# Kernel tuning notes

Measured on AMD Instinct MI355X. Metric: run time of the kernel, lower is better.

## Reference

```python
import jax, jax.numpy as jnp
import numpy as np

# SOLO decoupled-head postprocessing config (TrainConfig)
GRIDS = (40, 36, 24, 16, 12)
STRIDES = (4.0, 8.0, 16.0, 32.0, 64.0)
NMS_PRE = 500
SCORE_THR = 0.1
MASK_THR = 0.005
UPDATE_THR = 0.001
SIGMA = 2.0
MAX_PER_IMG = 100
NUM_CLASSES = 80


def _cell_meta():
    """Per-flattened-cell metadata across the 5 FPN levels (static)."""
    trans_diff, seg_diff, num_grids, strides = [], [], [], []
    t, s = 0, 0
    for g, st in zip(GRIDS, STRIDES):
        n = g * g
        trans_diff.append(np.full(n, t, np.int32))
        seg_diff.append(np.full(n, s, np.int32))
        num_grids.append(np.full(n, g, np.int32))
        strides.append(np.full(n, st, np.float32))
        t += n
        s += g
    return (jnp.asarray(np.concatenate(trans_diff)),
            jnp.asarray(np.concatenate(seg_diff)),
            jnp.asarray(np.concatenate(num_grids)),
            jnp.asarray(np.concatenate(strides)))


def setup_inputs() -> dict:
    key = jax.random.key(0)
    k1, k2, k3 = jax.random.split(key, 3)
    n_cells = sum(g * g for g in GRIDS)   # 3872
    n_rows = sum(GRIDS)                   # 128
    H, W = 200, 304                        # stride-4 map of an 800x1216 image
    return {
        "cate_preds": jax.random.uniform(k1, (n_cells, NUM_CLASSES), jnp.float32),
        "seg_preds_x": jax.random.uniform(k2, (n_rows, H, W), jnp.float32),
        "seg_preds_y": jax.random.uniform(k3, (n_rows, H, W), jnp.float32),
        "ori_h": 427,
        "ori_w": 640,
    }


def _matrix_nms(hardf, labels, scores, sum_masks):
    """Matrix NMS with gaussian decay. hardf: [n, h, w] float, descending scores."""
    n = hardf.shape[0]
    flat = hardf.reshape(n, -1)                      # [n, h*w]
    inter = flat @ flat.T                            # [n, n] pairwise intersection
    union = sum_masks[None, :] + sum_masks[:, None] - inter
    iou = jnp.where(union > 0, inter / jnp.maximum(union, 1e-12), 0.0)
    tri = jnp.triu(jnp.ones((n, n), jnp.float32), 1)  # cols > rows (strict upper)
    same = (labels[None, :] == labels[:, None]) & (labels[:, None] >= 0)
    decay_iou = iou * tri * same.astype(jnp.float32)  # [n, n]
    comp = decay_iou.max(axis=0)                      # max IoU with higher-scored same-class
    decay_m = jnp.exp(-SIGMA * decay_iou ** 2)
    comp_m = jnp.exp(-SIGMA * comp[:, None] ** 2)     # compensate[i, j] = f(comp[i])
    coeff = (decay_m / comp_m).min(axis=0)            # [n]
    return scores * coeff


def reference(cate_preds, seg_preds_x, seg_preds_y, ori_h, ori_w):
    trans_diff, seg_diff, num_grids, strides = _cell_meta()
    C = cate_preds.shape[1]
    flat = cate_preds.reshape(-1)
    flat = jnp.where(flat > SCORE_THR, flat, -1.0)
    scores, idx = jax.lax.top_k(flat, NMS_PRE)        # fixed-size candidate set
    loc = idx // C
    labels = (idx % C).astype(jnp.int32)
    valid = scores > SCORE_THR

    td, sd = trans_diff[loc], seg_diff[loc]
    ng, st = num_grids[loc], strides[loc]
    y_inds = (loc - td) // ng + sd
    x_inds = (loc - td) % ng + sd

    soft = seg_preds_x[x_inds] * seg_preds_y[y_inds]  # [N, H, W]
    hard = soft > MASK_THR
    sum_masks = hard.sum(axis=(1, 2)).astype(jnp.float32)
    keep = valid & (sum_masks > st)
    seg_score = (soft * hard).sum(axis=(1, 2)) / jnp.maximum(sum_masks, 1e-6)
    scores = jnp.where(keep, scores * seg_score, 0.0)
    keepf = keep.astype(jnp.float32)
    hardf = hard.astype(jnp.float32) * keepf[:, None, None]
    sum_masks = sum_masks * keepf
    labels = jnp.where(keep, labels, -1)

    # descending sort (matrix NMS assumes descending scores)
    order = jnp.argsort(-scores)
    scores, labels = scores[order], labels[order]
    soft, hardf, sum_masks = soft[order], hardf[order], sum_masks[order]

    scores = _matrix_nms(hardf, labels, scores, sum_masks)
    scores = jnp.where(scores > UPDATE_THR, scores, 0.0)

    top_scores, top_idx = jax.lax.top_k(scores, MAX_PER_IMG)
    top_soft = soft[top_idx]                          # [100, H, W]
    top_labels = labels[top_idx]

    H, W = top_soft.shape[1], top_soft.shape[2]
    up = jax.image.resize(top_soft, (MAX_PER_IMG, H * 4, W * 4), method="bilinear")
    up = jax.image.resize(up, (MAX_PER_IMG, ori_h, ori_w), method="bilinear")
    seg_masks = (up > MASK_THR).astype(jnp.float32)
    return seg_masks, top_labels, top_scores
```

## Files before the change

### kernel.cpp

```cpp
#include <hip/hip_runtime.h>
#include <stdint.h>

typedef unsigned int u32;
typedef unsigned long long u64;

#define NCELLS  3872
#define NCLS    80
#define NFLAT   309760
#define NPRE    500
#define NPAD    512
#define HH      200
#define WW      304
#define NPIX    60800
#define NWORDS  950
#define MSTRIDE 960
#define MAXOUT  100
#define OH      427
#define OW      640
#define MH      800
#define MW      1216
#define MAXG    4096
#define MAXPAIRS 16384
#define OUT_LBL 27328000
#define OUT_SCR 27328100
#define ROWS_PER_BLK 2
#define NRBLK 214

#define S_THR 0.1f
#define M_THR 0.005f
#define U_THR 0.001f

#define OFF_HIST1   0u
#define OFF_META    263168u
#define ZERO_BYTES  263232u
#define OFF_CAND    263424u
#define OFF_RAW     296192u
#define OFF_LOC     298240u
#define OFF_LABEL   300288u
#define OFF_XIND    302336u
#define OFF_YIND    304384u
#define OFF_STRIDE  306432u
#define OFF_SMF     308480u
#define OFF_SCORE   310528u
#define OFF_LABELK  312576u
#define OFF_ORDER   314624u
#define OFF_SSCORE  316672u
#define OFF_TOPC    318720u
#define OFF_PAIRI   319232u
#define OFF_PAIRIOU 384768u
#define OFF_W1YT0   450304u
#define OFF_W1YA    453504u
#define OFF_W1YB    456704u
#define OFF_W1XT0   459904u
#define OFF_W1XA    464768u
#define OFF_W1XB    469632u
#define OFF_W2YS    474496u
#define OFF_W2YW    476224u
#define OFF_W2XS    483072u
#define OFF_W2XW    485632u
#define OFF_MASKS   495872u
#define OFF_MASKT   4335872u
#define OFF_PARTD   8227072u
#define WS_NEED     12118272u

#define P_U32(off) ((u32*)(ws + (off)))
#define P_I32(off) ((int*)(ws + (off)))
#define P_F32(off) ((float*)(ws + (off)))
#define P_U64(off) ((u64*)(ws + (off)))

__device__ __forceinline__ void levelMeta(int loc, int& td, int& sd, int& ng, float& st) {
  if (loc < 1600)      { td = 0;    sd = 0;   ng = 40; st = 4.f;  }
  else if (loc < 2896) { td = 1600; sd = 40;  ng = 36; st = 8.f;  }
  else if (loc < 3472) { td = 2896; sd = 76;  ng = 24; st = 16.f; }
  else if (loc < 3728) { td = 3472; sd = 100; ng = 16; st = 32.f; }
  else                 { td = 3728; sd = 116; ng = 12; st = 64.f; }
}

__device__ __forceinline__ u32 vbin(float v) {
  int b = (int)(v * 65536.0f);
  if (b > 65535) b = 65535;
  if (b < 0) b = 0;
  return (u32)b;
}

__device__ __forceinline__ u64 shflx64(u64 v, int m) {
  u32 lo = (u32)v, hi = (u32)(v >> 32);
  lo = (u32)__shfl_xor((int)lo, m);
  hi = (u32)__shfl_xor((int)hi, m);
  return (((u64)hi) << 32) | lo;
}

__global__ void kh1(const float* __restrict__ cate, char* __restrict__ ws) {
  int i = blockIdx.x * 256 + threadIdx.x;
  if (i >= NFLAT / 4) return;
  float4 v = ((const float4*)cate)[i];
  u32* h = P_U32(OFF_HIST1);
  if (v.x > S_THR) atomicAdd(&h[vbin(v.x)], 1u);
  if (v.y > S_THR) atomicAdd(&h[vbin(v.y)], 1u);
  if (v.z > S_THR) atomicAdd(&h[vbin(v.z)], 1u);
  if (v.w > S_THR) atomicAdd(&h[vbin(v.w)], 1u);
}

__global__ __launch_bounds__(1024) void kc1(char* __restrict__ ws) {
  __shared__ u32 cs[1024];
  __shared__ u32 sfx[1024];
  __shared__ int cbS;
  __shared__ u32 aboveS;
  int t = threadIdx.x;
  const u32* h = P_U32(OFF_HIST1);
  u32 s = 0;
  for (int b = 0; b < 64; b++) s += h[t * 64 + b];
  cs[t] = s; sfx[t] = s;
  if (t == 0) cbS = -1;
  __syncthreads();
  for (int off = 1; off < 1024; off <<= 1) {
    u32 v = (t + off < 1024) ? sfx[t + off] : 0u;
    __syncthreads();
    sfx[t] += v;
    __syncthreads();
  }
  u32 nxt = (t < 1023) ? sfx[t + 1] : 0u;
  if (sfx[t] >= NPRE && nxt < NPRE) { cbS = t; aboveS = nxt; }
  __syncthreads();
  u32* meta = P_U32(OFF_META);
  if (cbS < 0) {
    if (t == 0) { meta[0] = 0u; meta[1] = sfx[0]; meta[2] = 0u; }
    return;
  }
  int cb = cbS;
  if (t < 64) cs[t] = h[cb * 64 + t];
  __syncthreads();
  if (t == 0) {
    u32 cum = aboveS;
    u32 bin = (u32)(cb * 64);
    for (int b = 63; b >= 0; b--) {
      u32 hb = cs[b];
      if (cum + hb >= NPRE) { bin = (u32)(cb * 64 + b); break; }
      cum += hb;
    }
    meta[0] = bin; meta[1] = cum; meta[2] = bin;
  }
}

__global__ void kg(const float* __restrict__ cate, char* __restrict__ ws) {
  u32 key = P_U32(OFF_META)[2];
  int i = blockIdx.x * 256 + threadIdx.x;
  if (i >= NFLAT / 4) return;
  float4 v = ((const float4*)cate)[i];
  u64* cand = P_U64(OFF_CAND);
  u32* cntp = &P_U32(OFF_META)[3];
  #pragma unroll
  for (int q = 0; q < 4; q++) {
    float f = (q == 0) ? v.x : (q == 1) ? v.y : (q == 2) ? v.z : v.w;
    if (f > S_THR && vbin(f) >= key) {
      u32 pos = atomicAdd(cntp, 1u);
      if (pos < MAXG) cand[pos] = (((u64)__float_as_uint(f)) << 32) | (u32)(~(u32)(i * 4 + q));
    }
  }
}

__global__ __launch_bounds__(1024) void kselw(char* __restrict__ ws) {
  __shared__ u64 sk[MAXG];
  int tid = threadIdx.x;
  int G = (int)P_U32(OFF_META)[3]; if (G > MAXG) G = MAXG;
  int n = NPAD;
  while (n < G) n <<= 1;
  const u64* cand = P_U64(OFF_CAND);
  if (n == NPAD) {
    u64 key = (tid < NPAD) ? ((tid < G) ? cand[tid] : 0ull) : 0ull;
    for (int k = 2; k <= NPAD; k <<= 1) {
      for (int j = k >> 1; j > 0; j >>= 1) {
        bool up = ((tid & k) == 0);
        u64 other;
        if (j < 64) {
          other = shflx64(key, j);
        } else {
          if (tid < NPAD) sk[tid] = key;
          __syncthreads();
          other = sk[(tid ^ j) & (NPAD - 1)];
          __syncthreads();
        }
        bool takeMax = (((tid & j) == 0) == up);
        u64 nk = takeMax ? (key > other ? key : other) : (key < other ? key : other);
        if (tid < NPAD) key = nk;
      }
    }
    if (tid < NPAD) sk[tid] = key;
    __syncthreads();
  } else {
    for (int i = tid; i < n; i += 1024) sk[i] = (i < G) ? cand[i] : 0ull;
    __syncthreads();
    for (int k = 2; k <= n; k <<= 1) {
      for (int j = k >> 1; j > 0; j >>= 1) {
        for (int i = tid; i < n; i += 1024) {
          int l = i ^ j;
          if (l > i) {
            u64 a = sk[i], b = sk[l];
            bool sw = ((i & k) == 0) ? (a < b) : (a > b);
            if (sw) { sk[i] = b; sk[l] = a; }
          }
        }
        __syncthreads();
      }
    }
  }
  if (tid < NPAD) {
    float rawv = -1.f; int loc = 0, lab = -1, xi = 0, yi = 0; float st = 3.0e38f;
    if (tid < NPRE && tid < G) {
      u64 key = sk[tid];
      u32 b = (u32)(key >> 32);
      u32 idx = ~((u32)(key & 0xffffffffu));
      rawv = __uint_as_float(b);
      loc = (int)(idx / (u32)NCLS);
      lab = (int)(idx - (u32)loc * NCLS);
      int td, sd, ng; levelMeta(loc, td, sd, ng, st);
      int rel = loc - td;
      int row = rel / ng;
      yi = row + sd;
      xi = (rel - row * ng) + sd;
    }
    P_F32(OFF_RAW)[tid] = rawv;
    P_I32(OFF_LABEL)[tid] = lab;
    P_I32(OFF_XIND)[tid] = xi;
    P_I32(OFF_YIND)[tid] = yi;
    P_F32(OFF_STRIDE)[tid] = st;
    P_F32(OFF_SCORE)[tid] = 0.f;
    P_I32(OFF_LABELK)[tid] = -1;
    P_F32(OFF_SMF)[tid] = 0.f;
  }
  int t = tid;
  for (int r = t; r < MH; r += 1024) {
    float s1 = ((float)r + 0.5f) * 0.25f - 0.5f;
    int t0 = (int)floorf(s1);
    float f = s1 - (float)t0;
    float wa = 1.f - f, wb = f;
    bool ia = (t0 >= 0) && (t0 < HH);
    bool ib = ((t0 + 1) >= 0) && ((t0 + 1) < HH);
    float tw = (ia ? wa : 0.f) + (ib ? wb : 0.f);
    float na = ia ? (wa / tw) : 0.f;
    float nb = ib ? (wb / tw) : 0.f;
    int base; float A, B;
    if (t0 < 0) { base = 0; A = nb; B = 0.f; }
    else if (t0 >= HH - 1) { base = HH - 2; A = 0.f; B = na; }
    else { base = t0; A = na; B = nb; }
    P_I32(OFF_W1YT0)[r] = base;
    P_F32(OFF_W1YA)[r] = A;
    P_F32(OFF_W1YB)[r] = B;
  }
  for (int c = t; c < MW; c += 1024) {
    float s1 = ((float)c + 0.5f) * 0.25f - 0.5f;
    int t0 = (int)floorf(s1);
    float f = s1 - (float)t0;
    float wa = 1.f - f, wb = f;
    bool ia = (t0 >= 0) && (t0 < WW);
    bool ib = ((t0 + 1) >= 0) && ((t0 + 1) < WW);
    float tw = (ia ? wa : 0.f) + (ib ? wb : 0.f);
    float na = ia ? (wa / tw) : 0.f;
    float nb = ib ? (wb / tw) : 0.f;
    int base; float A, B;
    if (t0 < 0) { base = 0; A = nb; B = 0.f; }
    else if (t0 >= WW - 1) { base = WW - 2; A = 0.f; B = na; }
    else { base = t0; A = na; B = nb; }
    P_I32(OFF_W1XT0)[c] = base;
    P_F32(OFF_W1XA)[c] = A;
    P_F32(OFF_W1XB)[c] = B;
  }
  for (int o = t; o < OH; o += 1024) {
    const float inv = (float)(800.0 / 427.0);
    float s2 = ((float)o + 0.5f) * inv - 0.5f;
    int rA = (int)ceilf(s2 - inv);
    int rB = (int)floorf(s2 + inv);
    if (rA < 0) rA = 0;
    if (rB > MH - 1) rB = MH - 1;
    float tot = 0.f;
    for (int r = rA; r <= rB; r++) {
      float x = fabsf(s2 - (float)r) / inv;
      float w = 1.f - x; if (w < 0.f) w = 0.f;
      tot += w;
    }
    int base = rA; if (base > MH - 4) base = MH - 4;
    float o4[4] = {0.f, 0.f, 0.f, 0.f};
    for (int r = rA; r <= rB; r++) {
      float x = fabsf(s2 - (float)r) / inv;
      float w = 1.f - x; if (w < 0.f) w = 0.f;
      o4[r - base] += w / tot;
    }
    P_I32(OFF_W2YS)[o] = base;
    float* wp = P_F32(OFF_W2YW) + o * 4;
    wp[0] = o4[0]; wp[1] = o4[1]; wp[2] = o4[2]; wp[3] = o4[3];
  }
  for (int o = t; o < OW; o += 1024) {
    const float inv = (float)(1216.0 / 640.0);
    float s2 = ((float)o + 0.5f) * inv - 0.5f;
    int rA = (int)ceilf(s2 - inv);
    int rB = (int)floorf(s2 + inv);
    if (rA < 0) rA = 0;
    if (rB > MW - 1) rB = MW - 1;
    float tot = 0.f;
    for (int r = rA; r <= rB; r++) {
      float x = fabsf(s2 - (float)r) / inv;
      float w = 1.f - x; if (w < 0.f) w = 0.f;
      tot += w;
    }
    int base = rA; if (base > MW - 4) base = MW - 4;
    float o4[4] = {0.f, 0.f, 0.f, 0.f};
    for (int r = rA; r <= rB; r++) {
      float x = fabsf(s2 - (float)r) / inv;
      float w = 1.f - x; if (w < 0.f) w = 0.f;
      o4[r - base] += w / tot;
    }
    P_I32(OFF_W2XS)[o] = base;
    float* wp = P_F32(OFF_W2XW) + o * 4;
    wp[0] = o4[0]; wp[1] = o4[1]; wp[2] = o4[2]; wp[3] = o4[3];
  }
}

__global__ __launch_bounds__(256) void kmaskA(const float* __restrict__ segx, const float* __restrict__ segy,
                                              char* __restrict__ ws) {
  __shared__ float lx[128 * 64];
  __shared__ float ly[128 * 64];
  int w0 = blockIdx.x;
  int base = w0 << 6;
  int tid = threadIdx.x;
  for (int idx = tid; idx < 128 * 64; idx += 256) {
    int r = idx >> 6, col = idx & 63;
    int sw = col ^ (r & 63);
    lx[(r << 6) + sw] = segx[(size_t)r * NPIX + base + col];
    ly[(r << 6) + sw] = segy[(size_t)r * NPIX + base + col];
  }
  __syncthreads();
  const int* xind = P_I32(OFF_XIND);
  const int* yind = P_I32(OFF_YIND);
  u64* maskT = P_U64(OFF_MASKT) + (size_t)w0 * NPAD;
  double* partD = (double*)(ws + OFF_PARTD) + (size_t)w0 * NPAD;
  for (int c = tid; c < NPRE; c += 256) {
    int xi = xind[c], yi = yind[c];
    const float* rx = &lx[xi << 6];
    const float* ry = &ly[yi << 6];
    int xk = xi & 63, yk = yi & 63;
    u32 lo = 0, hi = 0;
    double sum = 0.0;
    #pragma unroll 8
    for (int p = 0; p < 32; p++) {
      float s = rx[p ^ xk] * ry[p ^ yk];
      if (s > M_THR) { lo |= (1u << p); sum += (double)s; }
    }
    #pragma unroll 8
    for (int p = 32; p < 64; p++) {
      float s = rx[p ^ xk] * ry[p ^ yk];
      if (s > M_THR) { hi |= (1u << (p - 32)); sum += (double)s; }
    }
    maskT[c] = (((u64)hi) << 32) | lo;
    partD[c] = sum;
  }
}

__global__ __launch_bounds__(256) void kmaskBT(char* __restrict__ ws) {
  __shared__ u64 tile[64][65];
  int b = blockIdx.x;
  int tid = threadIdx.x;
  if (b < NPRE) {
    __shared__ double cd[256];
    __shared__ int ci[256];
    int c = b;
    const u64* maskT = P_U64(OFF_MASKT);
    const double* partD = (const double*)(ws + OFF_PARTD);
    double ds = 0.0; int cnt = 0;
    for (int w = tid; w < NWORDS; w += 256) {
      ds += partD[(size_t)w * NPAD + c];
      cnt += (int)__popcll(maskT[(size_t)w * NPAD + c]);
    }
    cd[tid] = ds; ci[tid] = cnt;
    __syncthreads();
    for (int s2 = 128; s2 > 0; s2 >>= 1) {
      if (tid < s2) { ci[tid] += ci[tid + s2]; cd[tid] += cd[tid + s2]; }
      __syncthreads();
    }
    if (tid == 0) {
      float sm = (float)ci[0];
      float rawv = P_F32(OFF_RAW)[c];
      bool valid = rawv > S_THR;
      bool keep = valid && (sm > P_F32(OFF_STRIDE)[c]);
      float ssf = (float)cd[0];
      float segsc = ssf / fmaxf(sm, 1e-6f);
      P_F32(OFF_SCORE)[c] = keep ? (rawv * segsc) : 0.f;
      P_F32(OFF_SMF)[c] = keep ? sm : 0.f;
      P_I32(OFF_LABELK)[c] = keep ? P_I32(OFF_LABEL)[c] : -1;
    }
  } else {
    int q = b - NPRE;
    int w0 = (q % 15) << 6;
    int c0 = (q / 15) << 6;
    const u64* maskT = P_U64(OFF_MASKT);
    for (int idx = tid; idx < 64 * 64; idx += 256) {
      int rw = idx >> 6, cc = idx & 63;
      int w = w0 + rw;
      tile[rw][cc] = (w < NWORDS) ? maskT[(size_t)w * NPAD + (c0 + cc)] : 0ull;
    }
    __syncthreads();
    u64* masks = P_U64(OFF_MASKS);
    for (int idx = tid; idx < 64 * 64; idx += 256) {
      int rc = idx >> 6, wwi = idx & 63;
      int c = c0 + rc, w = w0 + wwi;
      if (c < NPRE && w < NWORDS) masks[(size_t)c * MSTRIDE + w] = tile[wwi][rc];
    }
  }
}

__global__ __launch_bounds__(256) void kmask(const float* __restrict__ segx, const float* __restrict__ segy,
                                             char* __restrict__ ws) {
  int c = blockIdx.x;
  int tid = threadIdx.x;
  int lane = tid & 63, wv = tid >> 6;
  const float* X = segx + (size_t)P_I32(OFF_XIND)[c] * NPIX;
  const float* Y = segy + (size_t)P_I32(OFF_YIND)[c] * NPIX;
  u64* mrow = P_U64(OFF_MASKS) + (size_t)c * MSTRIDE;
  int cnt = 0;
  double ssum = 0.0;
  for (int w0 = wv; w0 < NWORDS; w0 += 4) {
    int p = (w0 << 6) + lane;
    float s = X[p] * Y[p];
    bool b = s > M_THR;
    u64 bal = __ballot(b ? 1 : 0);
    if (lane == 0) mrow[w0] = bal;
    if (b) { cnt++; ssum += (double)s; }
  }
  __shared__ int ci[256];
  __shared__ double cd[256];
  ci[tid] = cnt; cd[tid] = ssum;
  __syncthreads();
  for (int s2 = 128; s2 > 0; s2 >>= 1) {
    if (tid < s2) { ci[tid] += ci[tid + s2]; cd[tid] += cd[tid + s2]; }
    __syncthreads();
  }
  if (tid == 0) {
    float sm = (float)ci[0];
    float rawv = P_F32(OFF_RAW)[c];
    bool valid = rawv > S_THR;
    bool keep = valid && (sm > P_F32(OFF_STRIDE)[c]);
    float ssf = (float)cd[0];
    float segsc = ssf / fmaxf(sm, 1e-6f);
    P_F32(OFF_SCORE)[c] = keep ? (rawv * segsc) : 0.f;
    P_F32(OFF_SMF)[c] = keep ? sm : 0.f;
    P_I32(OFF_LABELK)[c] = keep ? P_I32(OFF_LABEL)[c] : -1;
  }
}

__global__ __launch_bounds__(512) void ksp(char* __restrict__ ws) {
  __shared__ u64 sk[NPAD];
  __shared__ short slab[NPAD];
  __shared__ u32 scan[NPAD];
  int t = threadIdx.x;
  float sc = (t < NPRE) ? P_F32(OFF_SCORE)[t] : 0.f;
  u64 key = (((u64)__float_as_uint(sc)) << 32) | (u32)(NPAD - 1 - t);
  for (int k = 2; k <= NPAD; k <<= 1) {
    for (int j = k >> 1; j > 0; j >>= 1) {
      bool up = ((t & k) == 0);
      u64 other;
      if (j < 64) {
        other = shflx64(key, j);
      } else {
        sk[t] = key;
        __syncthreads();
        other = sk[t ^ j];
        __syncthreads();
      }
      bool takeMax = (((t & j) == 0) == up);
      key = takeMax ? (key > other ? key : other) : (key < other ? key : other);
    }
  }
  int ord = NPAD - 1 - (int)(key & 0xffffffffu);
  P_I32(OFF_ORDER)[t] = ord;
  P_F32(OFF_SSCORE)[t] = __uint_as_float((u32)(key >> 32));
  const int* labelK = P_I32(OFF_LABELK);
  int lab = (t < NPRE) ? labelK[ord] : -1;
  slab[t] = (short)lab;
  __syncthreads();
  u32 cnt = 0;
  if (lab >= 0) {
    short lj = (short)lab;
    for (int i = 0; i < t; i++) if (slab[i] == lj) cnt++;
  }
  scan[t] = cnt;
  __syncthreads();
  for (int off = 1; off < NPAD; off <<= 1) {
    u32 v = (t >= off) ? scan[t - off] : 0u;
    __syncthreads();
    scan[t] += v;
    __syncthreads();
  }
  if (t == NPAD - 1) {
    u32 tot = scan[t];
    P_U32(OFF_META)[4] = (tot > MAXPAIRS) ? MAXPAIRS : tot;
  }
  if (lab >= 0 && cnt) {
    u32 pos = scan[t] - cnt;
    short lj = (short)lab;
    u32* pairI = P_U32(OFF_PAIRI);
    for (int i = 0; i < t; i++) {
      if (slab[i] == lj) {
        if (pos < MAXPAIRS) pairI[pos] = (((u32)i) << 16) | (u32)t;
        pos++;
      }
    }
  }
}

__global__ __launch_bounds__(64) void kpiou(char* __restrict__ ws) {
  int P = (int)P_U32(OFF_META)[4]; if (P > MAXPAIRS) P = MAXPAIRS;
  const int* order = P_I32(OFF_ORDER);
  const float* smf = P_F32(OFF_SMF);
  const u64* masks = P_U64(OFF_MASKS);
  for (int p = blockIdx.x; p < P; p += gridDim.x) {
    u32 ij = P_U32(OFF_PAIRI)[p];
    int oi = order[ij >> 16];
    int oj = order[ij & 0xffffu];
    const u64* mi = masks + (size_t)oi * MSTRIDE;
    const u64* mj = masks + (size_t)oj * MSTRIDE;
    int inter = 0;
    for (int w = threadIdx.x; w < NWORDS; w += 64)
      inter += (int)__popcll(mi[w] & mj[w]);
    for (int off = 32; off > 0; off >>= 1)
      inter += __shfl_down(inter, off);
    if (threadIdx.x == 0) {
      float fi = (float)inter;
      float uni = (smf[oj] + smf[oi]) - fi;
      float iou = (uni > 0.f) ? (fi / fmaxf(uni, 1e-12f)) : 0.f;
      P_F32(OFF_PAIRIOU)[p] = iou;
    }
  }
}

__global__ __launch_bounds__(512) void knms(char* __restrict__ ws, float* __restrict__ out) {
  __shared__ int compI[NPAD];
  __shared__ int coefI[NPAD];
  __shared__ u64 sk[NPAD];
  int t = threadIdx.x;
  int P = (int)P_U32(OFF_META)[4]; if (P > MAXPAIRS) P = MAXPAIRS;
  const u32* pairI = P_U32(OFF_PAIRI);
  const float* pairIou = P_F32(OFF_PAIRIOU);
  const float* sscore = P_F32(OFF_SSCORE);
  const int* order = P_I32(OFF_ORDER);
  const int* labelK = P_I32(OFF_LABELK);
  int* topc = P_I32(OFF_TOPC);
  compI[t] = 0;
  coefI[t] = __float_as_int(1.0f);
  __syncthreads();
  for (int p = t; p < P; p += 512) {
    int j = (int)(pairI[p] & 0xffffu);
    atomicMax(&compI[j], __float_as_int(pairIou[p]));
  }
  __syncthreads();
  for (int p = t; p < P; p += 512) {
    u32 ij = pairI[p];
    int i = (int)(ij >> 16), j = (int)(ij & 0xffffu);
    float x = pairIou[p];
    float c = __int_as_float(compI[i]);
    float x2 = x * x, c2 = c * c;
    float r = (float)exp(-2.0 * ((double)x2 - (double)c2));
    atomicMin(&coefI[j], __float_as_int(r));
  }
  __syncthreads();
  float ns = 0.f;
  if (t < NPRE) {
    ns = sscore[t] * __int_as_float(coefI[t]);
    ns = (ns > U_THR) ? ns : 0.f;
  }
  u64 key = (((u64)__float_as_uint(ns)) << 32) | (u32)(NPAD - 1 - t);
  for (int k = 2; k <= NPAD; k <<= 1) {
    for (int j = k >> 1; j > 0; j >>= 1) {
      bool up = ((t & k) == 0);
      u64 other;
      if (j < 64) {
        other = shflx64(key, j);
      } else {
        sk[t] = key;
        __syncthreads();
        other = sk[t ^ j];
        __syncthreads();
      }
      bool takeMax = (((t & j) == 0) == up);
      key = takeMax ? (key > other ? key : other) : (key < other ? key : other);
    }
  }
  if (t < MAXOUT) {
    int pos = NPAD - 1 - (int)(key & 0xffffffffu);
    int cand = order[pos];
    topc[t] = cand;
    out[OUT_LBL + t] = (float)labelK[cand];
    out[OUT_SCR + t] = __uint_as_float((u32)(key >> 32));
  }
}

__global__ __launch_bounds__(256) void kout(const float* __restrict__ segx, const float* __restrict__ segy,
                                            char* __restrict__ ws, float* __restrict__ out) {
  __shared__ float t1s[6][WW];
  __shared__ float yrs[2][MW];
  int flat = blockIdx.x;
  int w = (flat & 7) * 2675 + (flat >> 3);
  int kk = w / NRBLK;
  int r2 = w - kk * NRBLK;
  int oy0 = r2 * ROWS_PER_BLK;
  int nrow = (oy0 + 1 < OH) ? 2 : 1;
  int tid = threadIdx.x;
  int cand = P_I32(OFF_TOPC)[kk];
  const float* X = segx + (size_t)P_I32(OFF_XIND)[cand] * NPIX;
  const float* Y = segy + (size_t)P_I32(OFF_YIND)[cand] * NPIX;
  const int* w2ys = P_I32(OFF_W2YS);
  int rb = w2ys[oy0];
  const int* w1yT0 = P_I32(OFF_W1YT0);
  const float* w1yA = P_F32(OFF_W1YA);
  const float* w1yB = P_F32(OFF_W1YB);
  for (int mr = 0; mr < 6; mr++) {
    int r = rb + mr; if (r > MH - 1) r = MH - 1;
    int t0 = w1yT0[r];
    float A = w1yA[r], B = w1yB[r];
    const float* X0 = X + t0 * WW;
    const float* Y0 = Y + t0 * WW;
    const float* X1 = X0 + WW;
    const float* Y1 = Y0 + WW;
    for (int u = tid; u < WW; u += 256) {
      float s0 = X0[u] * Y0[u];
      float s1 = X1[u] * Y1[u];
      t1s[mr][u] = fmaf(B, s1, A * s0);
    }
  }
  __syncthreads();
  const int* w1xT0 = P_I32(OFF_W1XT0);
  const float* w1xA = P_F32(OFF_W1XA);
  const float* w1xB = P_F32(OFF_W1XB);
  float4 wy0 = *(const float4*)(P_F32(OFF_W2YW) + oy0 * 4);
  int oy1 = (nrow == 2) ? (oy0 + 1) : oy0;
  float4 wy1 = *(const float4*)(P_F32(OFF_W2YW) + oy1 * 4);
  int off1 = w2ys[oy1] - rb;
  for (int cc = tid; cc < MW; cc += 256) {
    int u0 = w1xT0[cc];
    float xa = w1xA[cc], xb = w1xB[cc];
    float up0 = fmaf(xb, t1s[0][u0 + 1], xa * t1s[0][u0]);
    float up1 = fmaf(xb, t1s[1][u0 + 1], xa * t1s[1][u0]);
    float up2 = fmaf(xb, t1s[2][u0 + 1], xa * t1s[2][u0]);
    float up3 = fmaf(xb, t1s[3][u0 + 1], xa * t1s[3][u0]);
    float up4 = fmaf(xb, t1s[4][u0 + 1], xa * t1s[4][u0]);
    float up5 = fmaf(xb, t1s[5][u0 + 1], xa * t1s[5][u0]);
    float v0 = wy0.x * up0;
    v0 = fmaf(wy0.y, up1, v0);
    v0 = fmaf(wy0.z, up2, v0);
    v0 = fmaf(wy0.w, up3, v0);
    yrs[0][cc] = v0;
    if (nrow == 2) {
      float a, b2, c3, d;
      if (off1 == 1)      { a = up1; b2 = up2; c3 = up3; d = up4; }
      else if (off1 == 2) { a = up2; b2 = up3; c3 = up4; d = up5; }
      else                { a = up0; b2 = up1; c3 = up2; d = up3; }
      float v1 = wy1.x * a;
      v1 = fmaf(wy1.y, b2, v1);
      v1 = fmaf(wy1.z, c3, v1);
      v1 = fmaf(wy1.w, d, v1);
      yrs[1][cc] = v1;
    }
  }
  __syncthreads();
  const int* w2xS = P_I32(OFF_W2XS);
  size_t ob0 = ((size_t)kk * OH + oy0) * OW;
  size_t ob1 = ob0 + OW;
  for (int ox = tid; ox < OW; ox += 256) {
    int cb = w2xS[ox];
    float4 wx = *(const float4*)(P_F32(OFF_W2XW) + ox * 4);
    float a0 = wx.x * yrs[0][cb];
    a0 = fmaf(wx.y, yrs[0][cb + 1], a0);
    a0 = fmaf(wx.z, yrs[0][cb + 2], a0);
    a0 = fmaf(wx.w, yrs[0][cb + 3], a0);
    out[ob0 + ox] = (a0 > M_THR) ? 1.0f : 0.0f;
    if (nrow == 2) {
      float a1 = wx.x * yrs[1][cb];
      a1 = fmaf(wx.y, yrs[1][cb + 1], a1);
      a1 = fmaf(wx.z, yrs[1][cb + 2], a1);
      a1 = fmaf(wx.w, yrs[1][cb + 3], a1);
      out[ob1 + ox] = (a1 > M_THR) ? 1.0f : 0.0f;
    }
  }
}

extern "C" void kernel_launch(void* const* d_in, const int* in_sizes, int n_in,
                              void* d_out, int out_size, void* d_ws, size_t ws_size,
                              hipStream_t stream) {
  (void)in_sizes; (void)n_in; (void)out_size;
  const float* cate = (const float*)d_in[0];
  const float* segx = (const float*)d_in[1];
  const float* segy = (const float*)d_in[2];
  char* ws = (char*)d_ws;
  float* out = (float*)d_out;
  const bool bigws = (ws_size >= (size_t)WS_NEED);

  hipMemsetAsync(ws, 0, ZERO_BYTES, stream);

  dim3 gFlat4((NFLAT / 4 + 255) / 256);
  hipLaunchKernelGGL(kh1, gFlat4, dim3(256), 0, stream, cate, ws);
  hipLaunchKernelGGL(kc1, dim3(1), dim3(1024), 0, stream, ws);
  hipLaunchKernelGGL(kg, gFlat4, dim3(256), 0, stream, cate, ws);
  hipLaunchKernelGGL(kselw, dim3(1), dim3(1024), 0, stream, ws);
  if (bigws) {
    hipLaunchKernelGGL(kmaskA, dim3(NWORDS), dim3(256), 0, stream, segx, segy, ws);
    hipLaunchKernelGGL(kmaskBT, dim3(NPRE + 120), dim3(256), 0, stream, ws);
  } else {
    hipLaunchKernelGGL(kmask, dim3(NPRE), dim3(256), 0, stream, segx, segy, ws);
  }
  hipLaunchKernelGGL(ksp, dim3(1), dim3(512), 0, stream, ws);
  hipLaunchKernelGGL(kpiou, dim3(2048), dim3(64), 0, stream, ws);
  hipLaunchKernelGGL(knms, dim3(1), dim3(512), 0, stream, ws, out);
  hipLaunchKernelGGL(kout, dim3(MAXOUT * NRBLK), dim3(256), 0, stream, segx, segy, ws, out);
}
```

Before: 243.3 us.

## Fuse threshold, gather and sort into one kernel; dedupe row loads in upsampling

Merges the cutoff-bin kernel, the candidate gather kernel and the select/sort kernel into a single 1024-thread block. Candidates are now collected into shared memory with a shared atomic counter, which removes two launches and the global candidate round trip. The cost is that one block must now scan all 77k float4 of the score tensor on its own. Separately, the output upsampling kernel loads four distinct source rows once and reuses them for all six intermediate rows, instead of reloading two rows per intermediate row.

Result: slower. 264.3 us (+8.7%).

```diff
diff --git a/kernel.cpp b/kernel.cpp
--- a/kernel.cpp
+++ b/kernel.cpp
@@ -32,7 +32,7 @@
 
 #define OFF_HIST1   0u
 #define OFF_META    263168u
-#define ZERO_BYTES  263232u
+#define ZERO_BYTES  262144u
 #define OFF_CAND    263424u
 #define OFF_RAW     296192u
 #define OFF_LOC     298240u
@@ -101,73 +101,68 @@
   if (v.w > S_THR) atomicAdd(&h[vbin(v.w)], 1u);
 }
 
-__global__ __launch_bounds__(1024) void kc1(char* __restrict__ ws) {
+__global__ __launch_bounds__(1024) void kselw(const float* __restrict__ cate, char* __restrict__ ws) {
+  __shared__ u64 sk[MAXG];
   __shared__ u32 cs[1024];
   __shared__ u32 sfx[1024];
   __shared__ int cbS;
   __shared__ u32 aboveS;
-  int t = threadIdx.x;
+  __shared__ u32 gcnt;
+  __shared__ u32 cutS;
+  int tid = threadIdx.x;
   const u32* h = P_U32(OFF_HIST1);
   u32 s = 0;
-  for (int b = 0; b < 64; b++) s += h[t * 64 + b];
-  cs[t] = s; sfx[t] = s;
-  if (t == 0) cbS = -1;
+  for (int b = 0; b < 64; b++) s += h[tid * 64 + b];
+  sfx[tid] = s;
+  if (tid == 0) { cbS = -1; gcnt = 0; cutS = 0; }
   __syncthreads();
   for (int off = 1; off < 1024; off <<= 1) {
-    u32 v = (t + off < 1024) ? sfx[t + off] : 0u;
-    __syncthreads();
-    sfx[t] += v;
-    __syncthreads();
-  }
-  u32 nxt = (t < 1023) ? sfx[t + 1] : 0u;
-  if (sfx[t] >= NPRE && nxt < NPRE) { cbS = t; aboveS = nxt; }
-  __syncthreads();
-  u32* meta = P_U32(OFF_META);
-  if (cbS < 0) {
-    if (t == 0) { meta[0] = 0u; meta[1] = sfx[0]; meta[2] = 0u; }
-    return;
-  }
-  int cb = cbS;
-  if (t < 64) cs[t] = h[cb * 64 + t];
-  __syncthreads();
-  if (t == 0) {
-    u32 cum = aboveS;
-    u32 bin = (u32)(cb * 64);
-    for (int b = 63; b >= 0; b--) {
-      u32 hb = cs[b];
-      if (cum + hb >= NPRE) { bin = (u32)(cb * 64 + b); break; }
-      cum += hb;
-    }
-    meta[0] = bin; meta[1] = cum; meta[2] = bin;
-  }
-}
-
-__global__ void kg(const float* __restrict__ cate, char* __restrict__ ws) {
-  u32 key = P_U32(OFF_META)[2];
-  int i = blockIdx.x * 256 + threadIdx.x;
-  if (i >= NFLAT / 4) return;
-  float4 v = ((const float4*)cate)[i];
-  u64* cand = P_U64(OFF_CAND);
-  u32* cntp = &P_U32(OFF_META)[3];
-  #pragma unroll
-  for (int q = 0; q < 4; q++) {
-    float f = (q == 0) ? v.x : (q == 1) ? v.y : (q == 2) ? v.z : v.w;
-    if (f > S_THR && vbin(f) >= key) {
-      u32 pos = atomicAdd(cntp, 1u);
-      if (pos < MAXG) cand[pos] = (((u64)__float_as_uint(f)) << 32) | (u32)(~(u32)(i * 4 + q));
-    }
-  }
-}
-
-__global__ __launch_bounds__(1024) void kselw(char* __restrict__ ws) {
-  __shared__ u64 sk[MAXG];
-  int tid = threadIdx.x;
-  int G = (int)P_U32(OFF_META)[3]; if (G > MAXG) G = MAXG;
+    u32 v = (tid + off < 1024) ? sfx[tid + off] : 0u;
+    __syncthreads();
+    sfx[tid] += v;
+    __syncthreads();
+  }
+  u32 nxt = (tid < 1023) ? sfx[tid + 1] : 0u;
+  if (sfx[tid] >= NPRE && nxt < NPRE) { cbS = tid; aboveS = nxt; }
+  __syncthreads();
+  if (cbS >= 0) {
+    int cb = cbS;
+    if (tid < 64) cs[tid] = h[cb * 64 + tid];
+    __syncthreads();
+    if (tid == 0) {
+      u32 cum = aboveS;
+      u32 bin = (u32)(cb * 64);
+      for (int b = 63; b >= 0; b--) {
+        u32 hb = cs[b];
+        if (cum + hb >= NPRE) { bin = (u32)(cb * 64 + b); break; }
+        cum += hb;
+      }
+      cutS = bin;
+    }
+  }
+  __syncthreads();
+  u32 cutbin = cutS;
+  const float4* cate4 = (const float4*)cate;
+  for (int i = tid; i < NFLAT / 4; i += 1024) {
+    float4 v = cate4[i];
+    #pragma unroll
+    for (int q = 0; q < 4; q++) {
+      float f = (q == 0) ? v.x : (q == 1) ? v.y : (q == 2) ? v.z : v.w;
+      if (f > S_THR && vbin(f) >= cutbin) {
+        u32 pos = atomicAdd(&gcnt, 1u);
+        if (pos < MAXG) sk[pos] = (((u64)__float_as_uint(f)) << 32) | (u32)(~(u32)(i * 4 + q));
+      }
+    }
+  }
+  __syncthreads();
+  int G = (int)gcnt; if (G > MAXG) G = MAXG;
   int n = NPAD;
   while (n < G) n <<= 1;
-  const u64* cand = P_U64(OFF_CAND);
+  for (int i = G + tid; i < n; i += 1024) sk[i] = 0ull;
+  __syncthreads();
   if (n == NPAD) {
-    u64 key = (tid < NPAD) ? ((tid < G) ? cand[tid] : 0ull) : 0ull;
+    u64 key = (tid < NPAD) ? sk[tid] : 0ull;
+    __syncthreads();
     for (int k = 2; k <= NPAD; k <<= 1) {
       for (int j = k >> 1; j > 0; j >>= 1) {
         bool up = ((tid & k) == 0);
@@ -188,8 +183,6 @@
     if (tid < NPAD) sk[tid] = key;
     __syncthreads();
   } else {
-    for (int i = tid; i < n; i += 1024) sk[i] = (i < G) ? cand[i] : 0ull;
-    __syncthreads();
     for (int k = 2; k <= n; k <<= 1) {
       for (int j = k >> 1; j > 0; j >>= 1) {
         for (int i = tid; i < n; i += 1024) {
@@ -205,13 +198,13 @@
     }
   }
   if (tid < NPAD) {
-    float rawv = -1.f; int loc = 0, lab = -1, xi = 0, yi = 0; float st = 3.0e38f;
+    float rawv = -1.f; int lab = -1, xi = 0, yi = 0; float st = 3.0e38f;
     if (tid < NPRE && tid < G) {
       u64 key = sk[tid];
       u32 b = (u32)(key >> 32);
       u32 idx = ~((u32)(key & 0xffffffffu));
       rawv = __uint_as_float(b);
-      loc = (int)(idx / (u32)NCLS);
+      int loc = (int)(idx / (u32)NCLS);
       lab = (int)(idx - (u32)loc * NCLS);
       int td, sd, ng; levelMeta(loc, td, sd, ng, st);
       int rel = loc - td;
@@ -611,18 +604,38 @@
   const int* w1yT0 = P_I32(OFF_W1YT0);
   const float* w1yA = P_F32(OFF_W1YA);
   const float* w1yB = P_F32(OFF_W1YB);
+  int smin = w1yT0[rb];
+  float Ay[6], By[6]; int i0a[6];
+  #pragma unroll
   for (int mr = 0; mr < 6; mr++) {
     int r = rb + mr; if (r > MH - 1) r = MH - 1;
-    int t0 = w1yT0[r];
-    float A = w1yA[r], B = w1yB[r];
-    const float* X0 = X + t0 * WW;
-    const float* Y0 = Y + t0 * WW;
-    const float* X1 = X0 + WW;
-    const float* Y1 = Y0 + WW;
+    i0a[mr] = w1yT0[r] - smin;
+    Ay[mr] = w1yA[r];
+    By[mr] = w1yB[r];
+  }
+  {
+    int r0 = smin;     if (r0 > HH - 1) r0 = HH - 1;
+    int r1 = smin + 1; if (r1 > HH - 1) r1 = HH - 1;
+    int r2s = smin + 2; if (r2s > HH - 1) r2s = HH - 1;
+    int r3 = smin + 3; if (r3 > HH - 1) r3 = HH - 1;
+    const float* X0 = X + r0 * WW; const float* Y0 = Y + r0 * WW;
+    const float* X1 = X + r1 * WW; const float* Y1 = Y + r1 * WW;
+    const float* X2 = X + r2s * WW; const float* Y2 = Y + r2s * WW;
+    const float* X3 = X + r3 * WW; const float* Y3 = Y + r3 * WW;
     for (int u = tid; u < WW; u += 256) {
       float s0 = X0[u] * Y0[u];
       float s1 = X1[u] * Y1[u];
-      t1s[mr][u] = fmaf(B, s1, A * s0);
+      float s2 = X2[u] * Y2[u];
+      float s3 = X3[u] * Y3[u];
+      #pragma unroll
+      for (int mr = 0; mr < 6; mr++) {
+        int i0 = i0a[mr];
+        float sa, sb;
+        if (i0 == 0)      { sa = s0; sb = s1; }
+        else if (i0 == 1) { sa = s1; sb = s2; }
+        else              { sa = s2; sb = s3; }
+        t1s[mr][u] = fmaf(By[mr], sb, Ay[mr] * sa);
+      }
     }
   }
   __syncthreads();
@@ -696,9 +709,7 @@
 
   dim3 gFlat4((NFLAT / 4 + 255) / 256);
   hipLaunchKernelGGL(kh1, gFlat4, dim3(256), 0, stream, cate, ws);
-  hipLaunchKernelGGL(kc1, dim3(1), dim3(1024), 0, stream, ws);
-  hipLaunchKernelGGL(kg, gFlat4, dim3(256), 0, stream, cate, ws);
-  hipLaunchKernelGGL(kselw, dim3(1), dim3(1024), 0, stream, ws);
+  hipLaunchKernelGGL(kselw, dim3(1), dim3(1024), 0, stream, cate, ws);
   if (bigws) {
     hipLaunchKernelGGL(kmaskA, dim3(NWORDS), dim3(256), 0, stream, segx, segy, ws);
     hipLaunchKernelGGL(kmaskBT, dim3(NPRE + 120), dim3(256), 0, stream, ws);
```
